# Kernel tuning notes

Measured on AMD Instinct MI355X. Metric: run time of the kernel, lower is better.

## Reference

```python
import jax, jax.numpy as jnp
import numpy as np

P, V, GRID = 64, 6890, 32
V_SUB = 256          # vertex subsample for the SDF-grid proxy
SCALE_FACTOR = 0.2   # forward() default
SDF_BAND = 0.15      # proxy: phi = relu(band - dist_to_surface) >= 0
N_FACES = 13776


def _trilinear(vol, pts):
    """torch grid_sample 3D, mode=bilinear, padding=zeros, align_corners=False.
    vol: [D,H,W]; pts: [...,3] with (x,y,z) in [-1,1] mapping to (W,H,D)."""
    D, H, W = vol.shape
    x = ((pts[..., 0] + 1.0) * W - 1.0) * 0.5
    y = ((pts[..., 1] + 1.0) * H - 1.0) * 0.5
    z = ((pts[..., 2] + 1.0) * D - 1.0) * 0.5
    x0 = jnp.floor(x).astype(jnp.int32); fx = x - x0
    y0 = jnp.floor(y).astype(jnp.int32); fy = y - y0
    z0 = jnp.floor(z).astype(jnp.int32); fz = z - z0

    def corner(xi, yi, zi, w):
        inb = (xi >= 0) & (xi < W) & (yi >= 0) & (yi < H) & (zi >= 0) & (zi < D)
        v = vol[jnp.clip(zi, 0, D - 1), jnp.clip(yi, 0, H - 1), jnp.clip(xi, 0, W - 1)]
        return jnp.where(inb, v, 0.0) * w

    return (corner(x0,     y0,     z0,     (1 - fx) * (1 - fy) * (1 - fz))
          + corner(x0 + 1, y0,     z0,     fx       * (1 - fy) * (1 - fz))
          + corner(x0,     y0 + 1, z0,     (1 - fx) * fy       * (1 - fz))
          + corner(x0 + 1, y0 + 1, z0,     fx       * fy       * (1 - fz))
          + corner(x0,     y0,     z0 + 1, (1 - fx) * (1 - fy) * fz)
          + corner(x0 + 1, y0,     z0 + 1, fx       * (1 - fy) * fz)
          + corner(x0,     y0 + 1, z0 + 1, (1 - fx) * fy       * fz)
          + corner(x0 + 1, y0 + 1, z0 + 1, fx       * fy       * fz))


def _compute_phi(verts_cs):
    """Deterministic non-negative SDF-grid proxy (stands in for the external
    SDF CUDA op; original computes it under no_grad). verts_cs: [P,V,3] in [-1,1].
    Returns phi: [P,GRID,GRID,GRID] (D,H,W indexing)."""
    # cell centers in normalized coords (align_corners=False convention)
    lin = (2.0 * jnp.arange(GRID, dtype=verts_cs.dtype) + 1.0) / GRID - 1.0
    zz, yy, xx = jnp.meshgrid(lin, lin, lin, indexing='ij')
    gp = jnp.stack([xx, yy, zz], axis=-1).reshape(-1, 3)  # [G^3,3] (x,y,z)
    stride = V // V_SUB
    sub = verts_cs[:, ::stride, :][:, :V_SUB]             # [P,V_SUB,3]

    def per_person(v):  # v: [V_SUB,3]
        d2 = jnp.sum((gp[:, None, :] - v[None, :, :]) ** 2, axis=-1)  # [G^3,V_SUB]
        d = jnp.sqrt(jnp.min(d2, axis=-1))
        return jnp.maximum(SDF_BAND - d, 0.0).reshape(GRID, GRID, GRID)

    return jax.lax.map(per_person, sub)  # sequential over people: bounds peak memory


def _forward(vertices, translation):
    sg = jax.lax.stop_gradient
    verts = vertices + translation[:, None, :]                      # [P,V,3]
    n = verts.shape[0]
    bmin = sg(jnp.min(verts, axis=1))                               # [P,3] (no_grad bboxes)
    bmax = sg(jnp.max(verts, axis=1))
    # overlap(i,j) per axis: not (min_i > max_j or min_j > max_i)
    ov = jnp.all((bmin[:, None, :] <= bmax[None, :, :]) &
                 (bmin[None, :, :] <= bmax[:, None, :]), axis=-1)   # [P,P], diag True
    # faithful to original ~filter_isolated_boxes: kept only if overlapping ALL others
    valid = jnp.all(ov, axis=1)                                     # [P]
    nv = jnp.sum(valid.astype(verts.dtype))
    center = (bmin + bmax) * 0.5                                    # [P,3]
    scale = (1.0 + SCALE_FACTOR) * 0.5 * jnp.max(bmax - bmin, axis=-1)  # [P]
    verts_cs = sg((verts - center[:, None, :]) / scale[:, None, None])
    phi = sg(_compute_phi(verts_cs))                                # [P,G,G,G]
    # coordinates of ALL people's vertices in person-i's grid frame: [P,P,V,3]
    loc = (verts[None, :, :, :] - center[:, None, None, :]) / scale[:, None, None, None]
    phi_val = jax.vmap(_trilinear)(phi, loc.reshape(n, n * V, 3)).reshape(n, n, V)
    # pair (i,j) contributes iff both valid and i != j (weights[i]=0 in the loop)
    pair_w = (valid[:, None] & valid[None, :] & ~jnp.eye(n, dtype=bool)).astype(verts.dtype)
    denom = jnp.maximum(nv, 1.0) ** 2
    return jnp.sum(pair_w * jnp.sum(phi_val, axis=-1)) / denom


def setup_inputs() -> dict:
    key = jax.random.key(0)
    k1, k2, k3 = jax.random.split(key, 3)
    vertices = jax.random.normal(k1, (P, V, 3), dtype=jnp.float32) * 0.2
    translation = jax.random.uniform(k2, (P, 3), dtype=jnp.float32, minval=-0.3, maxval=0.3)
    faces = jax.random.randint(k3, (N_FACES, 3), 0, V, dtype=jnp.int32)
    return {"vertices": vertices, "translation": translation, "faces": faces}


def reference(vertices, translation, faces):
    # faces only feed the external SDF op (replaced by the phi proxy); unused here
    return _forward(vertices, translation)
```

## Files before the change

kernel.cpp:

```cpp
#include <hip/hip_runtime.h>


#define NP 64
#define NVERT 6890
#define GRD 32
#define QDIM 34
#define QPLANE (QDIM*QDIM)
#define QVOL (QDIM*QPLANE)
#define VSUB 256
#define VSTRIDE 26
#define BAND 0.15f
#define PHI_SCALE 64.0f
#define INV_PHI_SCALE 0.015625f
#define LDS_BYTES (QVOL*2 + 128)
#define SAMPLE_BLOCKS (8*NP)

typedef float floatx2 __attribute__((ext_vector_type(2)));

__device__ __forceinline__ float wave_min(float v) {
  #pragma unroll
  for (int off = 32; off > 0; off >>= 1) v = fminf(v, __shfl_down(v, off));
  return v;
}
__device__ __forceinline__ float wave_max(float v) {
  #pragma unroll
  for (int off = 32; off > 0; off >>= 1) v = fmaxf(v, __shfl_down(v, off));
  return v;
}
__device__ __forceinline__ float wave_sum(float v) {
  #pragma unroll
  for (int off = 32; off > 0; off >>= 1) v += __shfl_down(v, off);
  return v;
}

__global__ __launch_bounds__(256) void k_soa_bounds(
    const float* __restrict__ verts, const float* __restrict__ trans,
    float* __restrict__ vertsT, float* __restrict__ bbox,
    float* __restrict__ accp, unsigned int* __restrict__ donep) {
  int p = blockIdx.x;
  if (p == 0 && threadIdx.x == 0) { accp[0] = 0.0f; donep[0] = 0u; }
  const float* vp = verts + (size_t)p * NVERT * 3;
  float tx = trans[p*3+0], ty = trans[p*3+1], tz = trans[p*3+2];
  float* o0 = vertsT + (size_t)(p*3+0) * NVERT;
  float* o1 = vertsT + (size_t)(p*3+1) * NVERT;
  float* o2 = vertsT + (size_t)(p*3+2) * NVERT;
  float mnx=1e30f, mny=1e30f, mnz=1e30f, mxx=-1e30f, mxy=-1e30f, mxz=-1e30f;
  for (int v = threadIdx.x; v < NVERT; v += blockDim.x) {
    float x = vp[v*3+0]+tx, y = vp[v*3+1]+ty, z = vp[v*3+2]+tz;
    o0[v] = x; o1[v] = y; o2[v] = z;
    mnx=fminf(mnx,x); mny=fminf(mny,y); mnz=fminf(mnz,z);
    mxx=fmaxf(mxx,x); mxy=fmaxf(mxy,y); mxz=fmaxf(mxz,z);
  }
  mnx=wave_min(mnx); mny=wave_min(mny); mnz=wave_min(mnz);
  mxx=wave_max(mxx); mxy=wave_max(mxy); mxz=wave_max(mxz);
  __shared__ float s[4][6];
  int wave = threadIdx.x >> 6, lane = threadIdx.x & 63;
  if (lane == 0) {
    s[wave][0]=mnx; s[wave][1]=mny; s[wave][2]=mnz;
    s[wave][3]=mxx; s[wave][4]=mxy; s[wave][5]=mxz;
  }
  __syncthreads();
  if (threadIdx.x == 0) {
    float a0=s[0][0],a1=s[0][1],a2=s[0][2],b0=s[0][3],b1=s[0][4],b2=s[0][5];
    for (int w = 1; w < 4; ++w) {
      a0=fminf(a0,s[w][0]); a1=fminf(a1,s[w][1]); a2=fminf(a2,s[w][2]);
      b0=fmaxf(b0,s[w][3]); b1=fmaxf(b1,s[w][4]); b2=fmaxf(b2,s[w][5]);
    }
    bbox[p*3+0]=a0; bbox[p*3+1]=a1; bbox[p*3+2]=a2;
    bbox[192+p*3+0]=b0; bbox[192+p*3+1]=b1; bbox[192+p*3+2]=b2;
  }
}

__global__ __launch_bounds__(1024) void k_phi(
    const float* __restrict__ verts, const float* __restrict__ trans,
    const float* __restrict__ bbox, unsigned short* __restrict__ pairs) {
  int p = blockIdx.x >> 2;
  int zq = blockIdx.x & 3;
  int tid = threadIdx.x;
  int x = tid & 31, y = tid >> 5;

  __shared__ float kv[VSUB][3];
  __shared__ float phib[8][32][32];
  __shared__ int nkeep;

  const float inv = 1.0f / (float)GRD;
  if (tid == 0) nkeep = 0;
  __syncthreads();

  float bx0 = bbox[p*3+0], by0 = bbox[p*3+1], bz0 = bbox[p*3+2];
  float bx1 = bbox[192+p*3+0], by1 = bbox[192+p*3+1], bz1 = bbox[192+p*3+2];
  float cx = 0.5f*(bx0+bx1), cy = 0.5f*(by0+by1), cz = 0.5f*(bz0+bz1);
  float ext = fmaxf(bx1-bx0, fmaxf(by1-by0, bz1-bz0));
  float is = 1.0f / (0.6f * ext);

  if (tid < VSUB) {
    int v = tid * VSTRIDE;
    const float* vp = verts + (size_t)p * NVERT * 3 + (size_t)v * 3;
    float X = (vp[0] + trans[p*3+0] - cx) * is;
    float Y = (vp[1] + trans[p*3+1] - cy) * is;
    float Z = (vp[2] + trans[p*3+2] - cz) * is;
    float zlo = (2.0f*(zq*8)     + 1.0f) * inv - 1.0f;
    float zhi = (2.0f*(zq*8 + 7) + 1.0f) * inv - 1.0f;
    float dz = fmaxf(fmaxf(zlo - Z, Z - zhi), 0.0f);
    if (dz < BAND) {
      int idx = atomicAdd(&nkeep, 1);
      kv[idx][0] = X; kv[idx][1] = Y; kv[idx][2] = Z;
    }
  }
  __syncthreads();
  int nk = nkeep;

  float gx = (2.0f*x + 1.0f) * inv - 1.0f;
  float gy = (2.0f*y + 1.0f) * inv - 1.0f;
  float gz[8];
  #pragma unroll
  for (int k = 0; k < 8; ++k) gz[k] = (2.0f*(zq*8+k) + 1.0f) * inv - 1.0f;

  float d2[8];
  #pragma unroll
  for (int k = 0; k < 8; ++k) d2[k] = 1e30f;

  int w = tid >> 6;
  float ylo = (4.0f*w + 1.0f) * inv - 1.0f;
  float yhi = (4.0f*w + 3.0f) * inv - 1.0f;

  for (int v = 0; v < nk; ++v) {
    float Y = kv[v][1];
    if (fmaxf(ylo - Y, Y - yhi) >= BAND) continue;
    float dx = gx - kv[v][0];
    float dy = gy - Y;
    float vz = kv[v][2];
    float r2 = fmaf(dy, dy, dx*dx);
    #pragma unroll
    for (int k = 0; k < 8; ++k) {
      float dz = gz[k] - vz;
      d2[k] = fminf(d2[k], fmaf(dz, dz, r2));
    }
  }
  #pragma unroll
  for (int k = 0; k < 8; ++k)
    phib[k][y][x] = fmaxf(BAND - sqrtf(d2[k]), 0.0f) * PHI_SCALE;
  __syncthreads();

  unsigned short* qp = pairs + (size_t)p * QVOL;
  for (int idx = tid; idx < QPLANE; idx += 1024) {
    int iy = idx / QDIM, ix = idx % QDIM;
    int gyy = iy - 1, gxx = ix - 1;
    bool gyok = (unsigned)gyy < 32u;
    bool aok = gyok && ((unsigned)gxx < 32u);
    bool bok = gyok && ((unsigned)ix  < 32u);
    int ya = gyok ? gyy : 0;
    int xa = aok ? gxx : 0;
    int xb = bok ? ix : 0;
    #pragma unroll
    for (int k = 0; k < 8; ++k) {
      float a = aok ? phib[k][ya][xa] : 0.0f;
      float b = bok ? phib[k][ya][xb] : 0.0f;
      int pk = __builtin_amdgcn_cvt_pk_fp8_f32(a, b, 0, false);
      qp[(zq*8 + k + 1)*QPLANE + idx] = (unsigned short)(pk & 0xffff);
    }
    if (zq == 0) qp[idx] = 0;
    if (zq == 3) qp[33*QPLANE + idx] = 0;
  }
}

__device__ __forceinline__ float qsample(const unsigned short* q,
                                         float X, float Y, float Z) {
  X = fminf(fmaxf(X, 0.0f), 33.99f);
  Y = fminf(fmaxf(Y, 0.0f), 32.999f);
  Z = fminf(fmaxf(Z, 0.0f), 32.999f);
  float xf = floorf(X), yf = floorf(Y), zf = floorf(Z);
  float fx = X - xf, fy = Y - yf, fz = Z - zf;
  int e = ((int)zf * QDIM + (int)yf) * QDIM + (int)xf;
  unsigned int w00 = q[e];
  unsigned int w10 = q[e + QDIM];
  unsigned int w01 = q[e + QPLANE];
  unsigned int w11 = q[e + QPLANE + QDIM];
  floatx2 c00 = __builtin_amdgcn_cvt_pk_f32_fp8((int)w00, false);
  floatx2 c10 = __builtin_amdgcn_cvt_pk_f32_fp8((int)w10, false);
  floatx2 c01 = __builtin_amdgcn_cvt_pk_f32_fp8((int)w01, false);
  floatx2 c11 = __builtin_amdgcn_cvt_pk_f32_fp8((int)w11, false);
  float u00 = fmaf(fx, c00.y - c00.x, c00.x);
  float u10 = fmaf(fx, c10.y - c10.x, c10.x);
  float u01 = fmaf(fx, c01.y - c01.x, c01.x);
  float u11 = fmaf(fx, c11.y - c11.x, c11.x);
  float a0 = fmaf(fy, u10 - u00, u00);
  float a1 = fmaf(fy, u11 - u01, u01);
  return fmaf(fz, a1 - a0, a0);
}

__global__ __launch_bounds__(896, 7) void k_sample(
    const float* __restrict__ vertsT, const float* __restrict__ bbox,
    const unsigned short* __restrict__ pairs, float* __restrict__ accp,
    unsigned int* __restrict__ donep, float* __restrict__ out) {
  extern __shared__ unsigned char smem[];
  const unsigned short* sq = (const unsigned short*)smem;
  float* red = (float*)(smem + (size_t)QVOL * 2);
  unsigned long long* maskp = (unsigned long long*)(smem + (size_t)QVOL*2 + 64);

  int i = blockIdx.y;
  int tid = threadIdx.x;

  float* sbb = (float*)smem;
  if (tid < 384) sbb[tid] = bbox[tid];
  __syncthreads();

  if (tid < 64) {
    const float* smn = sbb;
    const float* smx = sbb + 192;
    bool valid = true;
    for (int j = 0; j < NP; ++j) {
      bool ov = true;
      #pragma unroll
      for (int c = 0; c < 3; ++c)
        ov = ov && (smn[tid*3+c] <= smx[j*3+c]) && (smn[j*3+c] <= smx[tid*3+c]);
      valid = valid && ov;
    }
    unsigned long long mm = __ballot(valid);
    if (tid == 0) *maskp = mm;
  }
  float bx0 = sbb[i*3+0], by0 = sbb[i*3+1], bz0 = sbb[i*3+2];
  float bx1 = sbb[192+i*3+0], by1 = sbb[192+i*3+1], bz1 = sbb[192+i*3+2];
  float ext = fmaxf(bx1-bx0, fmaxf(by1-by0, bz1-bz0));
  float s16 = 16.0f / (0.6f * ext);
  float cx = 0.5f*(bx0+bx1), cy = 0.5f*(by0+by1), cz = 0.5f*(bz0+bz1);
  __syncthreads();
  unsigned long long mask = *maskp;

  bool active = (mask >> i) & 1ull;
  if (active) {
    const uint4* src = (const uint4*)(pairs + (size_t)i * QVOL);
    uint4* dst = (uint4*)smem;
    for (int t = tid; t < QVOL/8; t += 896) dst[t] = src[t];
    __syncthreads();

    int v = blockIdx.x * 896 + tid;
    bool ok = v < NVERT;
    int vc = ok ? v : 0;
    float bx = fmaf(-cx, s16, 16.5f) + (ok ? 0.0f : 1e9f);
    float by = fmaf(-cy, s16, 16.5f);
    float bz = fmaf(-cz, s16, 16.5f);

    float acc = 0.0f;
    unsigned long long m = mask & ~(1ull << i);
    while (m) {
      int jj = (int)__builtin_ctzll(m);
      m &= m - 1;
      const float* p0 = vertsT + (size_t)(jj*3) * NVERT;
      float X = fmaf(p0[vc],         s16, bx);
      float Y = fmaf(p0[NVERT+vc],   s16, by);
      float Z = fmaf(p0[2*NVERT+vc], s16, bz);
      acc += qsample(sq, X, Y, Z);
    }

    acc = wave_sum(acc);
    int wv = tid >> 6, lane = tid & 63;
    if (lane == 0) red[wv] = acc;
    __syncthreads();
    if (tid == 0) {
      float tot = 0.0f;
      #pragma unroll
      for (int w = 0; w < 14; ++w) tot += red[w];
      atomicAdd(accp, tot * INV_PHI_SCALE);
    }
  }

  if (tid == 0) {
    __threadfence();
    unsigned int old = atomicAdd(donep, 1u);
    if (old == SAMPLE_BLOCKS - 1) {
      float nv = fmaxf((float)__popcll(mask), 1.0f);
      float loss = atomicAdd(accp, 0.0f);
      out[0] = loss / (nv * nv);
    }
  }
}

extern "C" void kernel_launch(void* const* d_in, const int* in_sizes, int n_in,
                              void* d_out, int out_size, void* d_ws, size_t ws_size,
                              hipStream_t stream) {
  const float* verts = (const float*)d_in[0];
  const float* trans = (const float*)d_in[1];
  float* out = (float*)d_out;

  unsigned short* pairs = (unsigned short*)d_ws;
  float* vertsT    = (float*)((unsigned char*)d_ws + (size_t)NP * QVOL * 2);
  float* bbox      = vertsT + (size_t)NP * 3 * NVERT;
  float* accp      = bbox + 384;
  unsigned int* donep = (unsigned int*)(accp + 1);

  hipFuncSetAttribute((const void*)k_sample,
                      hipFuncAttributeMaxDynamicSharedMemorySize, LDS_BYTES);

  k_soa_bounds<<<NP, 256, 0, stream>>>(verts, trans, vertsT, bbox, accp, donep);
  k_phi<<<NP*4, 1024, 0, stream>>>(verts, trans, bbox, pairs);
  k_sample<<<dim3(8, NP), 896, LDS_BYTES, stream>>>(vertsT, bbox, pairs,
                                                    accp, donep, out);
}
```

Baseline: 119.3 us.

## Prefetch next partner vertices via LDS index list with interleaved vertex layout

```diff
diff --git a/kernel.cpp b/kernel.cpp
--- a/kernel.cpp
+++ b/kernel.cpp
@@ -3,6 +3,7 @@
 
 #define NP 64
 #define NVERT 6890
+#define NV3 (NVERT*3)
 #define GRD 32
 #define QDIM 34
 #define QPLANE (QDIM*QDIM)
@@ -12,7 +13,10 @@
 #define BAND 0.15f
 #define PHI_SCALE 64.0f
 #define INV_PHI_SCALE 0.015625f
-#define LDS_BYTES (QVOL*2 + 128)
+#define OFF_RED  (QVOL*2)
+#define OFF_MASK (QVOL*2 + 64)
+#define OFF_JL   (QVOL*2 + 80)
+#define LDS_BYTES (QVOL*2 + 224)
 #define SAMPLE_BLOCKS (8*NP)
 
 typedef float floatx2 __attribute__((ext_vector_type(2)));
@@ -35,19 +39,17 @@
 
 __global__ __launch_bounds__(256) void k_soa_bounds(
     const float* __restrict__ verts, const float* __restrict__ trans,
-    float* __restrict__ vertsT, float* __restrict__ bbox,
+    float* __restrict__ vertsA, float* __restrict__ bbox,
     float* __restrict__ accp, unsigned int* __restrict__ donep) {
   int p = blockIdx.x;
   if (p == 0 && threadIdx.x == 0) { accp[0] = 0.0f; donep[0] = 0u; }
-  const float* vp = verts + (size_t)p * NVERT * 3;
+  const float* vp = verts + (size_t)p * NV3;
+  float* op = vertsA + (size_t)p * NV3;
   float tx = trans[p*3+0], ty = trans[p*3+1], tz = trans[p*3+2];
-  float* o0 = vertsT + (size_t)(p*3+0) * NVERT;
-  float* o1 = vertsT + (size_t)(p*3+1) * NVERT;
-  float* o2 = vertsT + (size_t)(p*3+2) * NVERT;
   float mnx=1e30f, mny=1e30f, mnz=1e30f, mxx=-1e30f, mxy=-1e30f, mxz=-1e30f;
   for (int v = threadIdx.x; v < NVERT; v += blockDim.x) {
     float x = vp[v*3+0]+tx, y = vp[v*3+1]+ty, z = vp[v*3+2]+tz;
-    o0[v] = x; o1[v] = y; o2[v] = z;
+    op[v*3+0] = x; op[v*3+1] = y; op[v*3+2] = z;
     mnx=fminf(mnx,x); mny=fminf(mny,y); mnz=fminf(mnz,z);
     mxx=fmaxf(mxx,x); mxy=fmaxf(mxy,y); mxz=fmaxf(mxz,z);
   }
@@ -95,7 +97,7 @@
 
   if (tid < VSUB) {
     int v = tid * VSTRIDE;
-    const float* vp = verts + (size_t)p * NVERT * 3 + (size_t)v * 3;
+    const float* vp = verts + (size_t)p * NV3 + (size_t)v * 3;
     float X = (vp[0] + trans[p*3+0] - cx) * is;
     float Y = (vp[1] + trans[p*3+1] - cy) * is;
     float Z = (vp[2] + trans[p*3+2] - cz) * is;
@@ -190,13 +192,14 @@
 }
 
 __global__ __launch_bounds__(896, 7) void k_sample(
-    const float* __restrict__ vertsT, const float* __restrict__ bbox,
+    const float* __restrict__ vertsA, const float* __restrict__ bbox,
     const unsigned short* __restrict__ pairs, float* __restrict__ accp,
     unsigned int* __restrict__ donep, float* __restrict__ out) {
   extern __shared__ unsigned char smem[];
   const unsigned short* sq = (const unsigned short*)smem;
-  float* red = (float*)(smem + (size_t)QVOL * 2);
-  unsigned long long* maskp = (unsigned long long*)(smem + (size_t)QVOL*2 + 64);
+  float* red = (float*)(smem + OFF_RED);
+  unsigned long long* maskp = (unsigned long long*)(smem + OFF_MASK);
+  unsigned short* sjl = (unsigned short*)(smem + OFF_JL);
 
   int i = blockIdx.y;
   int tid = threadIdx.x;
@@ -218,6 +221,11 @@
     }
     unsigned long long mm = __ballot(valid);
     if (tid == 0) *maskp = mm;
+    unsigned long long mj = mm & ~(1ull << i);
+    if (valid && tid != i) {
+      int pos = (int)__popcll(mj & ((1ull << tid) - 1ull));
+      sjl[pos] = (unsigned short)tid;
+    }
   }
   float bx0 = sbb[i*3+0], by0 = sbb[i*3+1], bz0 = sbb[i*3+2];
   float bx1 = sbb[192+i*3+0], by1 = sbb[192+i*3+1], bz1 = sbb[192+i*3+2];
@@ -228,7 +236,8 @@
   unsigned long long mask = *maskp;
 
   bool active = (mask >> i) & 1ull;
-  if (active) {
+  int cnt = (int)__popcll(mask & ~(1ull << i));
+  if (active && cnt > 0) {
     const uint4* src = (const uint4*)(pairs + (size_t)i * QVOL);
     uint4* dst = (uint4*)smem;
     for (int t = tid; t < QVOL/8; t += 896) dst[t] = src[t];
@@ -236,21 +245,24 @@
 
     int v = blockIdx.x * 896 + tid;
     bool ok = v < NVERT;
-    int vc = ok ? v : 0;
+    int vc3 = (ok ? v : 0) * 3;
     float bx = fmaf(-cx, s16, 16.5f) + (ok ? 0.0f : 1e9f);
     float by = fmaf(-cy, s16, 16.5f);
     float bz = fmaf(-cz, s16, 16.5f);
 
     float acc = 0.0f;
-    unsigned long long m = mask & ~(1ull << i);
-    while (m) {
-      int jj = (int)__builtin_ctzll(m);
-      m &= m - 1;
-      const float* p0 = vertsT + (size_t)(jj*3) * NVERT;
-      float X = fmaf(p0[vc],         s16, bx);
-      float Y = fmaf(p0[NVERT+vc],   s16, by);
-      float Z = fmaf(p0[2*NVERT+vc], s16, bz);
-      acc += qsample(sq, X, Y, Z);
+    int jj = __builtin_amdgcn_readfirstlane((int)sjl[0]);
+    const float* pj = vertsA + (size_t)jj * NV3 + vc3;
+    float x0 = pj[0], y0 = pj[1], z0 = pj[2];
+    #pragma unroll 2
+    for (int t = 0; t < cnt; ++t) {
+      int tn = (t + 1 < cnt) ? t + 1 : t;
+      int jn = __builtin_amdgcn_readfirstlane((int)sjl[tn]);
+      const float* pn = vertsA + (size_t)jn * NV3 + vc3;
+      float xn = pn[0], yn = pn[1], zn = pn[2];
+      acc += qsample(sq, fmaf(x0, s16, bx), fmaf(y0, s16, by),
+                     fmaf(z0, s16, bz));
+      x0 = xn; y0 = yn; z0 = zn;
     }
 
     acc = wave_sum(acc);
@@ -284,16 +296,16 @@
   float* out = (float*)d_out;
 
   unsigned short* pairs = (unsigned short*)d_ws;
-  float* vertsT    = (float*)((unsigned char*)d_ws + (size_t)NP * QVOL * 2);
-  float* bbox      = vertsT + (size_t)NP * 3 * NVERT;
+  float* vertsA    = (float*)((unsigned char*)d_ws + (size_t)NP * QVOL * 2);
+  float* bbox      = vertsA + (size_t)NP * NV3;
   float* accp      = bbox + 384;
   unsigned int* donep = (unsigned int*)(accp + 1);
 
   hipFuncSetAttribute((const void*)k_sample,
                       hipFuncAttributeMaxDynamicSharedMemorySize, LDS_BYTES);
 
-  k_soa_bounds<<<NP, 256, 0, stream>>>(verts, trans, vertsT, bbox, accp, donep);
+  k_soa_bounds<<<NP, 256, 0, stream>>>(verts, trans, vertsA, bbox, accp, donep);
   k_phi<<<NP*4, 1024, 0, stream>>>(verts, trans, bbox, pairs);
-  k_sample<<<dim3(8, NP), 896, LDS_BYTES, stream>>>(vertsT, bbox, pairs,
+  k_sample<<<dim3(8, NP), 896, LDS_BYTES, stream>>>(vertsA, bbox, pairs,
                                                     accp, donep, out);
 }
```

Measured after the change: 118.1 us. About the same (-1.0%).

## Fuse bounds kernel into phi kernel and sample AoS vertices directly

Applied to the files above, without the earlier changes.

```diff
diff --git a/kernel.cpp b/kernel.cpp
--- a/kernel.cpp
+++ b/kernel.cpp
@@ -3,6 +3,7 @@
 
 #define NP 64
 #define NVERT 6890
+#define NV3 (NVERT*3)
 #define GRD 32
 #define QDIM 34
 #define QPLANE (QDIM*QDIM)
@@ -12,7 +13,7 @@
 #define BAND 0.15f
 #define PHI_SCALE 64.0f
 #define INV_PHI_SCALE 0.015625f
-#define LDS_BYTES (QVOL*2 + 128)
+#define LDS_BYTES (QVOL*2 + 64)
 #define SAMPLE_BLOCKS (8*NP)
 
 typedef float floatx2 __attribute__((ext_vector_type(2)));
@@ -33,47 +34,10 @@
   return v;
 }
 
-__global__ __launch_bounds__(256) void k_soa_bounds(
-    const float* __restrict__ verts, const float* __restrict__ trans,
-    float* __restrict__ vertsT, float* __restrict__ bbox,
-    float* __restrict__ accp, unsigned int* __restrict__ donep) {
-  int p = blockIdx.x;
-  if (p == 0 && threadIdx.x == 0) { accp[0] = 0.0f; donep[0] = 0u; }
-  const float* vp = verts + (size_t)p * NVERT * 3;
-  float tx = trans[p*3+0], ty = trans[p*3+1], tz = trans[p*3+2];
-  float* o0 = vertsT + (size_t)(p*3+0) * NVERT;
-  float* o1 = vertsT + (size_t)(p*3+1) * NVERT;
-  float* o2 = vertsT + (size_t)(p*3+2) * NVERT;
-  float mnx=1e30f, mny=1e30f, mnz=1e30f, mxx=-1e30f, mxy=-1e30f, mxz=-1e30f;
-  for (int v = threadIdx.x; v < NVERT; v += blockDim.x) {
-    float x = vp[v*3+0]+tx, y = vp[v*3+1]+ty, z = vp[v*3+2]+tz;
-    o0[v] = x; o1[v] = y; o2[v] = z;
-    mnx=fminf(mnx,x); mny=fminf(mny,y); mnz=fminf(mnz,z);
-    mxx=fmaxf(mxx,x); mxy=fmaxf(mxy,y); mxz=fmaxf(mxz,z);
-  }
-  mnx=wave_min(mnx); mny=wave_min(mny); mnz=wave_min(mnz);
-  mxx=wave_max(mxx); mxy=wave_max(mxy); mxz=wave_max(mxz);
-  __shared__ float s[4][6];
-  int wave = threadIdx.x >> 6, lane = threadIdx.x & 63;
-  if (lane == 0) {
-    s[wave][0]=mnx; s[wave][1]=mny; s[wave][2]=mnz;
-    s[wave][3]=mxx; s[wave][4]=mxy; s[wave][5]=mxz;
-  }
-  __syncthreads();
-  if (threadIdx.x == 0) {
-    float a0=s[0][0],a1=s[0][1],a2=s[0][2],b0=s[0][3],b1=s[0][4],b2=s[0][5];
-    for (int w = 1; w < 4; ++w) {
-      a0=fminf(a0,s[w][0]); a1=fminf(a1,s[w][1]); a2=fminf(a2,s[w][2]);
-      b0=fmaxf(b0,s[w][3]); b1=fmaxf(b1,s[w][4]); b2=fmaxf(b2,s[w][5]);
-    }
-    bbox[p*3+0]=a0; bbox[p*3+1]=a1; bbox[p*3+2]=a2;
-    bbox[192+p*3+0]=b0; bbox[192+p*3+1]=b1; bbox[192+p*3+2]=b2;
-  }
-}
-
 __global__ __launch_bounds__(1024) void k_phi(
     const float* __restrict__ verts, const float* __restrict__ trans,
-    const float* __restrict__ bbox, unsigned short* __restrict__ pairs) {
+    unsigned short* __restrict__ pairs, float* __restrict__ bbox,
+    float* __restrict__ accp, unsigned int* __restrict__ donep) {
   int p = blockIdx.x >> 2;
   int zq = blockIdx.x & 3;
   int tid = threadIdx.x;
@@ -81,24 +45,53 @@
 
   __shared__ float kv[VSUB][3];
   __shared__ float phib[8][32][32];
+  __shared__ float s[16][6];
+  __shared__ float bbf[6];
   __shared__ int nkeep;
 
+  if (blockIdx.x == 0 && tid == 0) { accp[0] = 0.0f; donep[0] = 0u; }
+
+  const float* vp = verts + (size_t)p * NV3;
+  float tx = trans[p*3+0], ty = trans[p*3+1], tz = trans[p*3+2];
+  float mnx=1e30f, mny=1e30f, mnz=1e30f, mxx=-1e30f, mxy=-1e30f, mxz=-1e30f;
+  for (int v = tid; v < NVERT; v += 1024) {
+    float xx = vp[v*3+0]+tx, yy = vp[v*3+1]+ty, zz = vp[v*3+2]+tz;
+    mnx=fminf(mnx,xx); mny=fminf(mny,yy); mnz=fminf(mnz,zz);
+    mxx=fmaxf(mxx,xx); mxy=fmaxf(mxy,yy); mxz=fmaxf(mxz,zz);
+  }
+  mnx=wave_min(mnx); mny=wave_min(mny); mnz=wave_min(mnz);
+  mxx=wave_max(mxx); mxy=wave_max(mxy); mxz=wave_max(mxz);
+  int wave = tid >> 6, lane = tid & 63;
+  if (lane == 0) {
+    s[wave][0]=mnx; s[wave][1]=mny; s[wave][2]=mnz;
+    s[wave][3]=mxx; s[wave][4]=mxy; s[wave][5]=mxz;
+  }
+  __syncthreads();
+  if (tid == 0) {
+    float a0=s[0][0],a1=s[0][1],a2=s[0][2],b0=s[0][3],b1=s[0][4],b2=s[0][5];
+    for (int w = 1; w < 16; ++w) {
+      a0=fminf(a0,s[w][0]); a1=fminf(a1,s[w][1]); a2=fminf(a2,s[w][2]);
+      b0=fmaxf(b0,s[w][3]); b1=fmaxf(b1,s[w][4]); b2=fmaxf(b2,s[w][5]);
+    }
+    bbf[0]=a0; bbf[1]=a1; bbf[2]=a2; bbf[3]=b0; bbf[4]=b1; bbf[5]=b2;
+    bbox[p*3+0]=a0; bbox[p*3+1]=a1; bbox[p*3+2]=a2;
+    bbox[192+p*3+0]=b0; bbox[192+p*3+1]=b1; bbox[192+p*3+2]=b2;
+    nkeep = 0;
+  }
+  __syncthreads();
+
+  float cx = 0.5f*(bbf[0]+bbf[3]), cy = 0.5f*(bbf[1]+bbf[4]);
+  float cz = 0.5f*(bbf[2]+bbf[5]);
+  float ext = fmaxf(bbf[3]-bbf[0], fmaxf(bbf[4]-bbf[1], bbf[5]-bbf[2]));
+  float is = 1.0f / (0.6f * ext);
   const float inv = 1.0f / (float)GRD;
-  if (tid == 0) nkeep = 0;
-  __syncthreads();
-
-  float bx0 = bbox[p*3+0], by0 = bbox[p*3+1], bz0 = bbox[p*3+2];
-  float bx1 = bbox[192+p*3+0], by1 = bbox[192+p*3+1], bz1 = bbox[192+p*3+2];
-  float cx = 0.5f*(bx0+bx1), cy = 0.5f*(by0+by1), cz = 0.5f*(bz0+bz1);
-  float ext = fmaxf(bx1-bx0, fmaxf(by1-by0, bz1-bz0));
-  float is = 1.0f / (0.6f * ext);
 
   if (tid < VSUB) {
     int v = tid * VSTRIDE;
-    const float* vp = verts + (size_t)p * NVERT * 3 + (size_t)v * 3;
-    float X = (vp[0] + trans[p*3+0] - cx) * is;
-    float Y = (vp[1] + trans[p*3+1] - cy) * is;
-    float Z = (vp[2] + trans[p*3+2] - cz) * is;
+    const float* vv = vp + (size_t)v * 3;
+    float X = (vv[0] + tx - cx) * is;
+    float Y = (vv[1] + ty - cy) * is;
+    float Z = (vv[2] + tz - cz) * is;
     float zlo = (2.0f*(zq*8)     + 1.0f) * inv - 1.0f;
     float zhi = (2.0f*(zq*8 + 7) + 1.0f) * inv - 1.0f;
     float dz = fmaxf(fmaxf(zlo - Z, Z - zhi), 0.0f);
@@ -190,48 +183,43 @@
 }
 
 __global__ __launch_bounds__(896, 7) void k_sample(
-    const float* __restrict__ vertsT, const float* __restrict__ bbox,
-    const unsigned short* __restrict__ pairs, float* __restrict__ accp,
-    unsigned int* __restrict__ donep, float* __restrict__ out) {
+    const float* __restrict__ verts, const float* __restrict__ trans,
+    const float* __restrict__ bbox, const unsigned short* __restrict__ pairs,
+    float* __restrict__ accp, unsigned int* __restrict__ donep,
+    float* __restrict__ out) {
   extern __shared__ unsigned char smem[];
   const unsigned short* sq = (const unsigned short*)smem;
   float* red = (float*)(smem + (size_t)QVOL * 2);
-  unsigned long long* maskp = (unsigned long long*)(smem + (size_t)QVOL*2 + 64);
 
   int i = blockIdx.y;
   int tid = threadIdx.x;
-
-  float* sbb = (float*)smem;
-  if (tid < 384) sbb[tid] = bbox[tid];
-  __syncthreads();
-
-  if (tid < 64) {
-    const float* smn = sbb;
-    const float* smx = sbb + 192;
-    bool valid = true;
-    for (int j = 0; j < NP; ++j) {
-      bool ov = true;
-      #pragma unroll
-      for (int c = 0; c < 3; ++c)
-        ov = ov && (smn[tid*3+c] <= smx[j*3+c]) && (smn[j*3+c] <= smx[tid*3+c]);
-      valid = valid && ov;
-    }
-    unsigned long long mm = __ballot(valid);
-    if (tid == 0) *maskp = mm;
-  }
-  float bx0 = sbb[i*3+0], by0 = sbb[i*3+1], bz0 = sbb[i*3+2];
-  float bx1 = sbb[192+i*3+0], by1 = sbb[192+i*3+1], bz1 = sbb[192+i*3+2];
+  int lane = tid & 63;
+
+  float amn0 = bbox[lane*3+0], amn1 = bbox[lane*3+1], amn2 = bbox[lane*3+2];
+  float amx0 = bbox[192+lane*3+0], amx1 = bbox[192+lane*3+1],
+        amx2 = bbox[192+lane*3+2];
+  bool valid = true;
+  for (int j = 0; j < NP; ++j) {
+    valid = valid && (amn0 <= bbox[192+j*3+0]) && (bbox[j*3+0] <= amx0)
+                  && (amn1 <= bbox[192+j*3+1]) && (bbox[j*3+1] <= amx1)
+                  && (amn2 <= bbox[192+j*3+2]) && (bbox[j*3+2] <= amx2);
+  }
+  unsigned long long mask = __ballot(valid);
+  int nvi = (int)__popcll(mask);
+  bool active = (mask >> i) & 1ull;
+
+  float bx0 = bbox[i*3+0], by0 = bbox[i*3+1], bz0 = bbox[i*3+2];
+  float bx1 = bbox[192+i*3+0], by1 = bbox[192+i*3+1], bz1 = bbox[192+i*3+2];
   float ext = fmaxf(bx1-bx0, fmaxf(by1-by0, bz1-bz0));
   float s16 = 16.0f / (0.6f * ext);
   float cx = 0.5f*(bx0+bx1), cy = 0.5f*(by0+by1), cz = 0.5f*(bz0+bz1);
-  __syncthreads();
-  unsigned long long mask = *maskp;
-
-  bool active = (mask >> i) & 1ull;
-  if (active) {
-    const uint4* src = (const uint4*)(pairs + (size_t)i * QVOL);
-    uint4* dst = (uint4*)smem;
-    for (int t = tid; t < QVOL/8; t += 896) dst[t] = src[t];
+
+  if (active && nvi > 1) {
+    {
+      const uint4* src = (const uint4*)(pairs + (size_t)i * QVOL);
+      uint4* dst = (uint4*)smem;
+      for (int t = tid; t < QVOL/8; t += 896) dst[t] = src[t];
+    }
     __syncthreads();
 
     int v = blockIdx.x * 896 + tid;
@@ -242,19 +230,20 @@
     float bz = fmaf(-cz, s16, 16.5f);
 
     float acc = 0.0f;
-    unsigned long long m = mask & ~(1ull << i);
-    while (m) {
-      int jj = (int)__builtin_ctzll(m);
-      m &= m - 1;
-      const float* p0 = vertsT + (size_t)(jj*3) * NVERT;
-      float X = fmaf(p0[vc],         s16, bx);
-      float Y = fmaf(p0[NVERT+vc],   s16, by);
-      float Z = fmaf(p0[2*NVERT+vc], s16, bz);
-      acc += qsample(sq, X, Y, Z);
+    #pragma unroll 2
+    for (int jj = 0; jj < NP; ++jj) {
+      if (jj == i || !((mask >> jj) & 1ull)) continue;
+      const float* vj = verts + ((size_t)jj * NVERT + vc) * 3;
+      float vx = vj[0], vy = vj[1], vz = vj[2];
+      float oxj = fmaf(trans[jj*3+0], s16, bx);
+      float oyj = fmaf(trans[jj*3+1], s16, by);
+      float ozj = fmaf(trans[jj*3+2], s16, bz);
+      acc += qsample(sq, fmaf(vx, s16, oxj), fmaf(vy, s16, oyj),
+                     fmaf(vz, s16, ozj));
     }
 
     acc = wave_sum(acc);
-    int wv = tid >> 6, lane = tid & 63;
+    int wv = tid >> 6;
     if (lane == 0) red[wv] = acc;
     __syncthreads();
     if (tid == 0) {
@@ -269,7 +258,7 @@
     __threadfence();
     unsigned int old = atomicAdd(donep, 1u);
     if (old == SAMPLE_BLOCKS - 1) {
-      float nv = fmaxf((float)__popcll(mask), 1.0f);
+      float nv = fmaxf((float)nvi, 1.0f);
       float loss = atomicAdd(accp, 0.0f);
       out[0] = loss / (nv * nv);
     }
@@ -284,16 +273,14 @@
   float* out = (float*)d_out;
 
   unsigned short* pairs = (unsigned short*)d_ws;
-  float* vertsT    = (float*)((unsigned char*)d_ws + (size_t)NP * QVOL * 2);
-  float* bbox      = vertsT + (size_t)NP * 3 * NVERT;
+  float* bbox      = (float*)((unsigned char*)d_ws + (size_t)NP * QVOL * 2);
   float* accp      = bbox + 384;
   unsigned int* donep = (unsigned int*)(accp + 1);
 
   hipFuncSetAttribute((const void*)k_sample,
                       hipFuncAttributeMaxDynamicSharedMemorySize, LDS_BYTES);
 
-  k_soa_bounds<<<NP, 256, 0, stream>>>(verts, trans, vertsT, bbox, accp, donep);
-  k_phi<<<NP*4, 1024, 0, stream>>>(verts, trans, bbox, pairs);
-  k_sample<<<dim3(8, NP), 896, LDS_BYTES, stream>>>(vertsT, bbox, pairs,
+  k_phi<<<NP*4, 1024, 0, stream>>>(verts, trans, pairs, bbox, accp, donep);
+  k_sample<<<dim3(8, NP), 896, LDS_BYTES, stream>>>(verts, trans, bbox, pairs,
                                                     accp, donep, out);
 }
```

New measurement: 118.3 us. About the same (-0.8%).
